# Kernel optimization log

Hardware: AMD Instinct MI355X
Metric: run time of the kernel (lower is better)

Reference implementation:

```python
import jax, jax.numpy as jnp
import numpy as np

B, S1, S2, H = 8, 2048, 2048, 1024

def setup_inputs() -> dict:
    key = jax.random.key(0)
    k1, k2, kw, kb = jax.random.split(key, 4)
    hidden1 = jax.random.normal(k1, (B, S1, H), dtype=jnp.float32)
    hidden2 = jax.random.normal(k2, (B, S2, H), dtype=jnp.float32)
    W = jax.random.normal(kw, (H, H), dtype=jnp.float32) * 0.001
    bias = jax.random.normal(kb, (1,), dtype=jnp.float32) * 0.02
    return {"hidden1": hidden1, "hidden2": hidden2, "W": W, "bias": bias}

def reference(hidden1, hidden2, W, bias):
    # weight[b, i, j] = (hidden1 @ W)[b, i, :] . hidden2[b, j, :] + bias
    weight = jnp.einsum('bih,hk,bjk->bij', hidden1, W, hidden2) + bias[0]  # (B, S1, S2)
    # softmax over s1 (dim=1), then transpose-bmm with hidden1 -> (B, S2, H)
    a1 = jax.nn.softmax(weight, axis=1)
    hidden_1 = jnp.einsum('bij,bih->bjh', a1, hidden1)
    # softmax over s2 (dim=2), bmm with hidden2 -> (B, S1, H)
    a2 = jax.nn.softmax(weight, axis=2)
    hidden_2 = jnp.einsum('bij,bjh->bih', a2, hidden2)
    return (hidden_1, hidden_2)
```

## Files before the change

### kernel.cpp

```cpp
#include <hip/hip_runtime.h>
#include <stdint.h>

#define B_  8
#define S1_ 2048
#define S2_ 2048
#define H_  1024

typedef __attribute__((ext_vector_type(8))) short bf16x8;
typedef __attribute__((ext_vector_type(4))) float f32x4;
typedef unsigned short u16;

__device__ __forceinline__ u16 f2bf(float f){
  union { float f; uint32_t v; } x; x.f = f;
  uint32_t r = x.v + 0x7fffu + ((x.v >> 16) & 1u);
  return (u16)(r >> 16);
}
__device__ __forceinline__ u16 f2h(float f){
  union { _Float16 h; u16 u; } c; c.h = (_Float16)f; return c.u;
}
__device__ __forceinline__ float h2f(u16 u){
  union { _Float16 h; u16 u; } c; c.u = u; return (float)c.h;
}
__device__ __forceinline__ uint32_t pk2bf(float lo, float hi){
  uint32_t r;
  asm("v_cvt_pk_bf16_f32 %0, %1, %2" : "=v"(r) : "v"(lo), "v"(hi));
  return r;
}
__device__ __forceinline__ void async16(void* lds, const void* g){
  __builtin_amdgcn_global_load_lds(
      (const __attribute__((address_space(1))) uint32_t*)g,
      (__attribute__((address_space(3))) uint32_t*)lds, 16, 0, 0);
}

__global__ __launch_bounds__(256) void k_cvt_bf16(const float* __restrict__ in,
                                                  u16* __restrict__ out, long n){
  long i = ((long)blockIdx.x * 256 + threadIdx.x) * 8;
  const long stride = (long)gridDim.x * 256 * 8;
  for (; i < n; i += stride){
    float4 a = *(const float4*)(in + i);
    float4 b = *(const float4*)(in + i + 4);
    union { bf16x8 v; uint32_t w[4]; } o;
    o.w[0] = pk2bf(a.x, a.y); o.w[1] = pk2bf(a.z, a.w);
    o.w[2] = pk2bf(b.x, b.y); o.w[3] = pk2bf(b.z, b.w);
    *(bf16x8*)(out + i) = o.v;
  }
}

__global__ __launch_bounds__(256) void k_tcvt(const float* __restrict__ in,
                                              u16* __restrict__ out, int R, int Cc){
  __shared__ u16 t[32][33];
  in  += (long)blockIdx.z * R * Cc;
  out += (long)blockIdx.z * R * Cc;
  const int x = threadIdx.x & 31, y0 = threadIdx.x >> 5;
  const int bx = blockIdx.x * 32, by = blockIdx.y * 32;
  for (int r = y0; r < 32; r += 8) t[r][x] = f2bf(in[(long)(by + r) * Cc + bx + x]);
  __syncthreads();
  for (int r = y0; r < 32; r += 8) out[(long)(bx + r) * R + by + x] = t[x][r];
}

__global__ __launch_bounds__(256) void k_cvtT2(const float* __restrict__ in,
                                               u16* __restrict__ out_n,
                                               u16* __restrict__ out_t, int R, int Cc){
  __shared__ u16 t[64][68];
  in    += (long)blockIdx.z * R * Cc;
  out_n += (long)blockIdx.z * R * Cc;
  out_t += (long)blockIdx.z * R * Cc;
  const int tid = threadIdx.x;
  const int r0 = tid >> 4;
  const int c4 = (tid & 15) * 4;
  const int bx = blockIdx.x * 64;
  const int by = blockIdx.y * 64;
#pragma unroll
  for (int it = 0; it < 4; ++it){
    const int r = it*16 + r0;
    float4 v = *(const float4*)(in + (long)(by + r)*Cc + bx + c4);
    u16 b0 = f2bf(v.x), b1 = f2bf(v.y), b2 = f2bf(v.z), b3 = f2bf(v.w);
    ushort4 o; o.x = b0; o.y = b1; o.z = b2; o.w = b3;
    *(ushort4*)(out_n + (long)(by + r)*Cc + bx + c4) = o;
    t[r][c4] = b0; t[r][c4+1] = b1; t[r][c4+2] = b2; t[r][c4+3] = b3;
  }
  __syncthreads();
#pragma unroll
  for (int it = 0; it < 4; ++it){
    const int c = it*16 + r0;
    ushort4 o;
    o.x = t[c4  ][c]; o.y = t[c4+1][c]; o.z = t[c4+2][c]; o.w = t[c4+3][c];
    *(ushort4*)(out_t + (long)(bx + c)*R + by + c4) = o;
  }
}

__global__ __launch_bounds__(256) void k_cvtT2m(
    const float* __restrict__ in1, u16* __restrict__ n1, u16* __restrict__ t1,
    const float* __restrict__ in2, u16* __restrict__ n2, u16* __restrict__ t2,
    int R, int Cc){
  __shared__ u16 t[64][68];
  const int zb = blockIdx.z & 7;
  const bool second = blockIdx.z >= 8;
  const float* in = (second ? in2 : in1) + (long)zb * R * Cc;
  u16* out_n = (second ? n2 : n1) + (long)zb * R * Cc;
  u16* out_t = (second ? t2 : t1) + (long)zb * R * Cc;
  const int tid = threadIdx.x;
  const int r0 = tid >> 4;
  const int c4 = (tid & 15) * 4;
  const int bx = blockIdx.x * 64;
  const int by = blockIdx.y * 64;
#pragma unroll
  for (int it = 0; it < 4; ++it){
    const int r = it*16 + r0;
    float4 v = *(const float4*)(in + (long)(by + r)*Cc + bx + c4);
    u16 b0 = f2bf(v.x), b1 = f2bf(v.y), b2 = f2bf(v.z), b3 = f2bf(v.w);
    ushort4 o; o.x = b0; o.y = b1; o.z = b2; o.w = b3;
    *(ushort4*)(out_n + (long)(by + r)*Cc + bx + c4) = o;
    t[r][c4] = b0; t[r][c4+1] = b1; t[r][c4+2] = b2; t[r][c4+3] = b3;
  }
  __syncthreads();
#pragma unroll
  for (int it = 0; it < 4; ++it){
    const int c = it*16 + r0;
    ushort4 o;
    o.x = t[c4  ][c]; o.y = t[c4+1][c]; o.z = t[c4+2][c]; o.w = t[c4+3][c];
    *(ushort4*)(out_t + (long)(bx + c)*R + by + c4) = o;
  }
}

template<int OM, bool STATS>
__global__ __launch_bounds__(512) void k_gemm256(
    const u16* __restrict__ A, const u16* __restrict__ Bm, void* __restrict__ Cv,
    int M, int N, int K, long sA, long sB, long sC,
    float* __restrict__ rpmax, float* __restrict__ rpsum,
    float* __restrict__ cpmax, float* __restrict__ cpsum)
{
  const int GX = gridDim.x, GY = gridDim.y;
  const long plane = (long)GX * GY;
  const long tot = plane * gridDim.z;
  const long lin = blockIdx.x + (long)GX * (blockIdx.y + (long)GY * blockIdx.z);
  const long chunk = tot >> 3;
  const long swz = (lin & 7) * chunk + (lin >> 3);
  const int bz = (int)(swz / plane);
  const int rr = (int)(swz % plane);
  const int by_ = rr / GX, bx_ = rr % GX;

  A += (long)bz * sA; Bm += (long)bz * sB;
  __shared__ u16 lds[2 * 32768];
  const int tid = threadIdx.x, lane = tid & 63, w = tid >> 6;
  const int wm = w >> 2, wn = w & 3;
  const int brow = bx_ * 256, bcol = by_ * 256;

  f32x4 acc[8][4];
#pragma unroll
  for (int m=0;m<8;++m)
#pragma unroll
    for (int n=0;n<4;++n) acc[m][n] = (f32x4){0.f,0.f,0.f,0.f};

  const int fr = lane & 15;
  const int hi = lane >> 4;
  const int sk0 = (((0*4)+hi) ^ (fr & 7)) * 8;
  const int sk1 = (((1*4)+hi) ^ (fr & 7)) * 8;

  const u16* gAs[4]; const u16* gBs[4];
#pragma unroll
  for (int j=0;j<4;++j){
    const int cc = (w*4 + j)*64 + lane;
    const int row = cc >> 3;
    const int sl = (cc & 7) ^ (row & 7);
    gAs[j] = A  + (long)(brow + row) * K + sl*8;
    gBs[j] = Bm + (long)(bcol + row) * K + sl*8;
  }
  auto stage = [&](int buf, int t){
    u16* base = lds + buf*32768;
#pragma unroll
    for (int j=0;j<4;++j) async16(base + (w*4+j)*512, gAs[j] + (long)t*64);
#pragma unroll
    for (int j=0;j<4;++j) async16(base + 16384 + (w*4+j)*512, gBs[j] + (long)t*64);
  };
  auto ldfragK = [&](int buf, int sk, bf16x8* a, bf16x8* b){
    const u16* At = lds + buf*32768;
    const u16* Bt = At + 16384;
#pragma unroll
    for (int n=0;n<4;++n) b[n] = *(const bf16x8*)(Bt + (wn*64 + n*16 + fr)*64 + sk);
#pragma unroll
    for (int m=0;m<8;++m) a[m] = *(const bf16x8*)(At + (wm*128 + m*16 + fr)*64 + sk);
  };

  const int NT = K >> 6;
  stage(0, 0);
  asm volatile("s_waitcnt vmcnt(0)" ::: "memory");
  __builtin_amdgcn_s_barrier();

  for (int t = 0; t < NT; ++t){
    const int cur = t & 1;
    if (t + 1 < NT) stage(cur ^ 1, t + 1);

    bf16x8 a[8], b[4];
    ldfragK(cur, sk0, a, b);
    __builtin_amdgcn_s_setprio(1);
#pragma unroll
    for (int m=0;m<8;++m)
#pragma unroll
      for (int n=0;n<4;++n)
        acc[m][n] = __builtin_amdgcn_mfma_f32_16x16x32_bf16(a[m], b[n], acc[m][n], 0,0,0);
    __builtin_amdgcn_s_setprio(0);

    ldfragK(cur, sk1, a, b);
    __builtin_amdgcn_s_setprio(1);
#pragma unroll
    for (int m=0;m<8;++m)
#pragma unroll
      for (int n=0;n<4;++n)
        acc[m][n] = __builtin_amdgcn_mfma_f32_16x16x32_bf16(a[m], b[n], acc[m][n], 0,0,0);
    __builtin_amdgcn_s_setprio(0);

    if (t + 1 < NT){
      asm volatile("s_waitcnt vmcnt(0)" ::: "memory");
      asm volatile("s_waitcnt lgkmcnt(0)" ::: "memory");
      __builtin_amdgcn_s_barrier();
    }
  }

  const int crow = brow + wm*128 + hi * 4;
  const int ccol = bcol + wn*64 + fr;
  if constexpr (OM == 2){
    float* C = (float*)Cv + (long)bz * sC;
#pragma unroll
    for (int m=0;m<8;++m)
#pragma unroll
      for (int n=0;n<4;++n){
        f32x4 v = acc[m][n];
        float* cp = C + (long)(crow + m*16) * N + ccol + n*16;
#pragma unroll
        for (int q=0;q<4;++q) cp[(long)q*N] = v[q];
      }
  } else {
    u16* C = (u16*)Cv + (long)bz * sC;
#pragma unroll
    for (int m=0;m<8;++m)
#pragma unroll
      for (int n=0;n<4;++n){
        f32x4 v = acc[m][n];
        u16* cp = C + (long)(crow + m*16) * N + ccol + n*16;
#pragma unroll
        for (int q=0;q<4;++q) cp[(long)q*N] = OM ? f2h(v[q]) : f2bf(v[q]);
      }
  }

  if constexpr (STATS){
#pragma unroll
    for (int m=0;m<8;++m){
      f32x4 mx = acc[m][0];
#pragma unroll
      for (int n=1;n<4;++n)
#pragma unroll
        for (int q=0;q<4;++q) mx[q] = fmaxf(mx[q], acc[m][n][q]);
#pragma unroll
      for (int off=1; off<16; off<<=1)
#pragma unroll
        for (int q=0;q<4;++q) mx[q] = fmaxf(mx[q], __shfl_xor(mx[q], off));
      f32x4 sm = (f32x4){0.f,0.f,0.f,0.f};
#pragma unroll
      for (int n=0;n<4;++n)
#pragma unroll
        for (int q=0;q<4;++q) sm[q] += __expf(acc[m][n][q] - mx[q]);
#pragma unroll
      for (int off=1; off<16; off<<=1)
#pragma unroll
        for (int q=0;q<4;++q) sm[q] += __shfl_xor(sm[q], off);
      if (fr == 0){
        const int nb = by_*4 + wn;
        const long rb = ((long)bz*32 + nb)*2048 + brow + wm*128 + m*16 + hi*4;
#pragma unroll
        for (int q=0;q<4;++q){ rpmax[rb+q] = mx[q]; rpsum[rb+q] = sm[q]; }
      }
    }
#pragma unroll
    for (int n=0;n<4;++n){
      float mx = acc[0][n][0];
#pragma unroll
      for (int m=0;m<8;++m)
#pragma unroll
        for (int q=0;q<4;++q) mx = fmaxf(mx, acc[m][n][q]);
      mx = fmaxf(mx, __shfl_xor(mx, 16));
      mx = fmaxf(mx, __shfl_xor(mx, 32));
      float sm = 0.f;
#pragma unroll
      for (int m=0;m<8;++m)
#pragma unroll
        for (int q=0;q<4;++q) sm += __expf(acc[m][n][q] - mx);
      sm += __shfl_xor(sm, 16);
      sm += __shfl_xor(sm, 32);
      if (hi == 0){
        const int mb = bx_*2 + wm;
        const long cb = ((long)bz*16 + mb)*2048 + bcol + wn*64 + n*16 + fr;
        cpmax[cb] = mx; cpsum[cb] = sm;
      }
    }
  }
}

__global__ __launch_bounds__(256) void k_combine(
    const float* __restrict__ rpmax, const float* __restrict__ rpsum,
    const float* __restrict__ cpmax, const float* __restrict__ cpsum,
    float* __restrict__ rmax, float* __restrict__ rinv,
    float* __restrict__ cmax, float* __restrict__ cinv)
{
  const long i = (long)blockIdx.x*256 + threadIdx.x;
  const int b = (int)(i >> 11), r = (int)(i & 2047);
  if (blockIdx.y == 0){
    const float* pm = rpmax + ((long)b*32)*2048 + r;
    const float* ps = rpsum + ((long)b*32)*2048 + r;
    float m = -3.4e38f;
#pragma unroll
    for (int k=0;k<32;++k) m = fmaxf(m, pm[(long)k*2048]);
    float s = 0.f;
#pragma unroll
    for (int k=0;k<32;++k) s += ps[(long)k*2048] * __expf(pm[(long)k*2048] - m);
    rmax[i] = m; rinv[i] = 1.f / s;
  } else {
    const float* pm = cpmax + ((long)b*16)*2048 + r;
    const float* ps = cpsum + ((long)b*16)*2048 + r;
    float m = -3.4e38f;
#pragma unroll
    for (int k=0;k<16;++k) m = fmaxf(m, pm[(long)k*2048]);
    float s = 0.f;
#pragma unroll
    for (int k=0;k<16;++k) s += ps[(long)k*2048] * __expf(pm[(long)k*2048] - m);
    cmax[i] = m; cinv[i] = 1.f / s;
  }
}

__global__ __launch_bounds__(256) void k_p1t2(u16* __restrict__ Wg, u16* __restrict__ P2,
                                              const float* __restrict__ cmax,
                                              const float* __restrict__ cinv,
                                              const float* __restrict__ rmax,
                                              const float* __restrict__ rinv){
  const int ti = blockIdx.x, tj = blockIdx.y;
  if (tj < ti) return;
  const int b = blockIdx.z;
  u16* S = Wg + (long)b * S1_ * S2_;
  u16* P2b = P2 ? P2 + (long)b * S1_ * S2_ : (u16*)nullptr;
  const int I0 = ti*64, J0 = tj*64;
  __shared__ u16 tA[64][68];
  __shared__ u16 tB[64][68];
  __shared__ float scm[128], sci[128];
  const int tid = threadIdx.x;
  if (tid < 64){ scm[tid] = cmax[b*S2_ + J0 + tid]; sci[tid] = cinv[b*S2_ + J0 + tid]; }
  else if (tid < 128){ scm[tid] = cmax[b*S2_ + I0 + tid - 64]; sci[tid] = cinv[b*S2_ + I0 + tid - 64]; }
  __syncthreads();

  const int r0 = tid >> 3;
  const int c8 = (tid & 7) * 8;
#pragma unroll
  for (int it = 0; it < 2; ++it){
    const int r = it*32 + r0;
    bf16x8 v = *(const bf16x8*)(S + (long)(I0 + r)*S2_ + J0 + c8);
    const float rm = rmax[b*S1_ + I0 + r], ri = rinv[b*S1_ + I0 + r];
    union { bf16x8 v; uint32_t w[4]; } p2o;
#pragma unroll
    for (int k=0;k<4;++k){
      float x0 = h2f((u16)v[2*k]), x1 = h2f((u16)v[2*k+1]);
      p2o.w[k] = pk2bf(__expf(x0 - rm)*ri, __expf(x1 - rm)*ri);
      tA[r][c8+2*k]   = f2bf(__expf(x0 - scm[c8+2*k])   * sci[c8+2*k]);
      tA[r][c8+2*k+1] = f2bf(__expf(x1 - scm[c8+2*k+1]) * sci[c8+2*k+1]);
    }
    if (P2b) *(bf16x8*)(P2b + (long)(I0 + r)*S2_ + J0 + c8) = p2o.v;
  }
  if (ti != tj){
#pragma unroll
    for (int it = 0; it < 2; ++it){
      const int r = it*32 + r0;
      bf16x8 v = *(const bf16x8*)(S + (long)(J0 + r)*S2_ + I0 + c8);
      const float rm = rmax[b*S1_ + J0 + r], ri = rinv[b*S1_ + J0 + r];
      union { bf16x8 v; uint32_t w[4]; } p2o;
#pragma unroll
      for (int k=0;k<4;++k){
        float x0 = h2f((u16)v[2*k]), x1 = h2f((u16)v[2*k+1]);
        p2o.w[k] = pk2bf(__expf(x0 - rm)*ri, __expf(x1 - rm)*ri);
        tB[r][c8+2*k]   = f2bf(__expf(x0 - scm[64+c8+2*k])   * sci[64+c8+2*k]);
        tB[r][c8+2*k+1] = f2bf(__expf(x1 - scm[64+c8+2*k+1]) * sci[64+c8+2*k+1]);
      }
      if (P2b) *(bf16x8*)(P2b + (long)(J0 + r)*S2_ + I0 + c8) = p2o.v;
    }
  }
  __syncthreads();
  const int rr = tid >> 4;
  const int c4 = (tid & 15) * 4;
#pragma unroll
  for (int it = 0; it < 4; ++it){
    const int c = it*16 + rr;
    ushort4 o;
    o.x = tA[c4  ][c]; o.y = tA[c4+1][c]; o.z = tA[c4+2][c]; o.w = tA[c4+3][c];
    *(ushort4*)(S + (long)(J0 + c)*S2_ + I0 + c4) = o;
  }
  if (ti != tj){
#pragma unroll
    for (int it = 0; it < 4; ++it){
      const int c = it*16 + rr;
      ushort4 o;
      o.x = tB[c4  ][c]; o.y = tB[c4+1][c]; o.z = tB[c4+2][c]; o.w = tB[c4+3][c];
      *(ushort4*)(S + (long)(I0 + c)*S2_ + J0 + c4) = o;
    }
  }
}

__global__ __launch_bounds__(256) void k_gemm_h2(
    const u16* __restrict__ Wg, const u16* __restrict__ Bt, float* __restrict__ C,
    const float* __restrict__ rmax, const float* __restrict__ rinv)
{
  const int b = blockIdx.z;
  const u16* A  = Wg + (long)b * S1_ * S2_;
  const u16* Bp = Bt + (long)b * H_ * S2_;
  float* Cp = C + (long)b * S1_ * H_;

  __shared__ u16 As[128*32];
  __shared__ u16 Bs[128*32];
  const int tid = threadIdx.x, lane = tid & 63, w = tid >> 6;
  const int wr = (w >> 1) * 64, wc = (w & 1) * 64;
  const int brow = blockIdx.x * 128, bcol = blockIdx.y * 128;
  f32x4 acc[4][4];
#pragma unroll
  for (int m=0;m<4;++m)
#pragma unroll
    for (int n=0;n<4;++n) acc[m][n] = (f32x4){0.f,0.f,0.f,0.f};

  const int arow = w*16 + (lane >> 2);
  const int scol = (lane & 3) * 8;
  const u16* gA0 = A + (long)(brow + arow) * S2_ + scol;
  const u16* gA1 = gA0 + (long)64 * S2_;
  const float rm0 = rmax[b*S1_ + brow + arow],      ri0 = rinv[b*S1_ + brow + arow];
  const float rm1 = rmax[b*S1_ + brow + arow + 64], ri1 = rinv[b*S1_ + brow + arow + 64];
  u16* wA0 = As + arow*32 + scol;
  u16* wA1 = As + (arow+64)*32 + scol;

  const u16* gb = Bp + (long)(bcol + arow) * S2_ + scol;
  u16* lB0 = Bs + (w*16)*32;  u16* lB1 = Bs + (64 + w*16)*32;

  const int koff = (lane >> 4) * 8;
  const int fr = lane & 15;

  for (int k0 = 0; k0 < S2_; k0 += 32){
    bf16x8 x0 = *(const bf16x8*)(gA0 + k0);
    bf16x8 x1 = *(const bf16x8*)(gA1 + k0);
    async16(lB0, gb);  async16(lB1, gb + (long)64*S2_);
    gb += 32;
    union { bf16x8 v; uint32_t w4[4]; } y0, y1;
#pragma unroll
    for (int k=0;k<4;++k){
      y0.w4[k] = pk2bf(__expf(h2f((u16)x0[2*k])   - rm0) * ri0,
                       __expf(h2f((u16)x0[2*k+1]) - rm0) * ri0);
      y1.w4[k] = pk2bf(__expf(h2f((u16)x1[2*k])   - rm1) * ri1,
                       __expf(h2f((u16)x1[2*k+1]) - rm1) * ri1);
    }
    *(bf16x8*)wA0 = y0.v;
    *(bf16x8*)wA1 = y1.v;
    __syncthreads();
    bf16x8 af[4], bf[4];
#pragma unroll
    for (int m=0;m<4;++m) af[m] = *(const bf16x8*)(As + (wr + m*16 + fr)*32 + koff);
#pragma unroll
    for (int n=0;n<4;++n) bf[n] = *(const bf16x8*)(Bs + (wc + n*16 + fr)*32 + koff);
#pragma unroll
    for (int m=0;m<4;++m)
#pragma unroll
      for (int n=0;n<4;++n)
        acc[m][n] = __builtin_amdgcn_mfma_f32_16x16x32_bf16(af[m], bf[n], acc[m][n], 0,0,0);
    __syncthreads();
  }
  const int crow = brow + wr + (lane >> 4) * 4;
  const int ccol = bcol + wc + fr;
#pragma unroll
  for (int m=0;m<4;++m)
#pragma unroll
    for (int n=0;n<4;++n){
      f32x4 v = acc[m][n];
      float* cp = Cp + (long)(crow + m*16) * H_ + ccol + n*16;
#pragma unroll
      for (int q=0;q<4;++q) cp[(long)q*H_] = v[q];
    }
}

extern "C" void kernel_launch(void* const* d_in, const int* in_sizes, int n_in,
                              void* d_out, int out_size, void* d_ws, size_t ws_size,
                              hipStream_t stream)
{
  const float* h1 = (const float*)d_in[0];
  const float* h2 = (const float*)d_in[1];
  const float* W  = (const float*)d_in[2];
  float* out0 = (float*)d_out;
  float* out1 = out0 + (size_t)B_ * S2_ * H_;

  const long NE = (long)B_ * S1_ * H_;
  const long NS = (long)B_ * S1_ * S2_;

  char* ws = (char*)d_ws;
  size_t off = 0;
  float* rmax = (float*)(ws + off); off += (size_t)B_*S1_*4;
  float* rinv = (float*)(ws + off); off += (size_t)B_*S1_*4;
  float* cmax = (float*)(ws + off); off += (size_t)B_*S2_*4;
  float* cinv = (float*)(ws + off); off += (size_t)B_*S2_*4;
  u16* Wg  = (u16*)(ws + off);
  u16* WTb = Wg;
  off += (size_t)NS*2;
  u16* h1t = (u16*)(ws + off); off += (size_t)NE*2;

  const bool use_p2 = ws_size >= off + (size_t)NS*2;
  u16* P2 = use_p2 ? (u16*)(ws + off) : (u16*)nullptr;
  size_t off2 = off + (use_p2 ? (size_t)NS*2 : 0);
  const bool ws_h2t = ws_size >= off2 + (size_t)NE*2;

  u16* h1b = (u16*)out0;
  u16* h2b = (u16*)out0 + NE;
  u16* h2t = ws_h2t ? (u16*)(ws + off2) : (u16*)out0;
  u16* Qb  = (u16*)out1;
  float* rpmax = (float*)((u16*)out1 + NE);
  float* rpsum = rpmax + (size_t)B_*32*2048;
  float* cpmax = rpsum + (size_t)B_*32*2048;
  float* cpsum = cpmax + (size_t)B_*16*2048;

  if (ws_h2t){
    k_cvtT2m<<<dim3(16,32,16), 256, 0, stream>>>(h1, h1b, h1t, h2, h2b, h2t, S1_, H_);
  } else {
    k_cvtT2<<<dim3(16,32,8), 256, 0, stream>>>(h1, h1b, h1t, S1_, H_);
    k_cvt_bf16<<<dim3(4096), 256, 0, stream>>>(h2, h2b, NE);
  }
  k_tcvt<<<dim3(32,32,1), 256, 0, stream>>>(W, WTb, H_, H_);
  k_gemm256<0,false><<<dim3(8, 4, 8), 512, 0, stream>>>(h1b, WTb, Qb, S1_, H_, H_,
        (long)S1_*H_, 0L, (long)S1_*H_, nullptr, nullptr, nullptr, nullptr);
  if (!ws_h2t){
    k_tcvt<<<dim3(32,64,8), 256, 0, stream>>>(h2, h2t, S2_, H_);
  }
  k_gemm256<1,true><<<dim3(8, 8, 8), 512, 0, stream>>>(Qb, h2b, Wg, S1_, S2_, H_,
        (long)S1_*H_, (long)S2_*H_, (long)S1_*S2_, rpmax, rpsum, cpmax, cpsum);
  k_combine<<<dim3(64, 2), 256, 0, stream>>>(rpmax, rpsum, cpmax, cpsum,
                                             rmax, rinv, cmax, cinv);
  if (use_p2){
    k_p1t2<<<dim3(32,32,8), 256, 0, stream>>>(Wg, P2, cmax, cinv, rmax, rinv);
    k_gemm256<2,false><<<dim3(8, 4, 8), 512, 0, stream>>>(P2, h2t, out1, S1_, H_, S2_,
          (long)S1_*S2_, (long)H_*S2_, (long)S1_*H_, nullptr, nullptr, nullptr, nullptr);
  } else {
    k_gemm_h2<<<dim3(16, 8, 8), 256, 0, stream>>>(Wg, h2t, out1, rmax, rinv);
    k_p1t2<<<dim3(32,32,8), 256, 0, stream>>>(Wg, (u16*)nullptr, cmax, cinv, rmax, rinv);
  }
  k_gemm256<2,false><<<dim3(8, 4, 8), 512, 0, stream>>>(Wg, h1t, out0, S2_, H_, S1_,
        (long)S1_*S2_, (long)H_*S1_, (long)S2_*H_, nullptr, nullptr, nullptr, nullptr);
}
```

Measured before the change: 355.2 us.

## Add 256x128-tile triple-buffered GEMM kernel for the H-output GEMMs

Adds a new GEMM kernel that uses a 256x128 output tile with 4x4 MFMA fragments per wave, a three-stage async LDS pipeline, and an XCD-aware block swizzle. The Q projection GEMM and both P@H output GEMMs now use it instead of the 256x256 kernel, which doubles the grid to 512 blocks. The aim is better CU occupancy and load balance across the 256 CUs, since the old grid of 256 blocks left none to spare. In exchange, each block loads more A-tile traffic per output element because reuse along N is lower.

```diff
diff --git a/kernel.cpp b/kernel.cpp
--- a/kernel.cpp
+++ b/kernel.cpp
@@ -293,6 +293,117 @@
         cpmax[cb] = mx; cpsum[cb] = sm;
       }
     }
+  }
+}
+
+template<int OM>
+__global__ __launch_bounds__(512, 4) void k_gemm128n(
+    const u16* __restrict__ A, const u16* __restrict__ Bm, void* __restrict__ Cv,
+    int M, int N, int K, long sA, long sB, long sC)
+{
+  const int GX = gridDim.x, GY = gridDim.y;
+  const long plane = (long)GX * GY;
+  const long tot = plane * gridDim.z;
+  const long lin = blockIdx.x + (long)GX * (blockIdx.y + (long)GY * blockIdx.z);
+  const long chunk = tot >> 3;
+  const long swz = (lin & 7) * chunk + (lin >> 3);
+  const int bz = (int)(swz / plane);
+  const int rr = (int)(swz % plane);
+  const int by_ = rr / GX, bx_ = rr % GX;
+
+  A += (long)bz * sA; Bm += (long)bz * sB;
+  __shared__ u16 lds[3 * 12288];
+  const int tid = threadIdx.x, lane = tid & 63, w = tid >> 6;
+  const int wm = w >> 1, wn = w & 1;
+  const int brow = bx_ * 256, bcol = by_ * 128;
+
+  f32x4 acc[4][4];
+#pragma unroll
+  for (int m=0;m<4;++m)
+#pragma unroll
+    for (int n=0;n<4;++n) acc[m][n] = (f32x4){0.f,0.f,0.f,0.f};
+
+  const int fr = lane & 15;
+  const int hi = lane >> 4;
+  const int g8s = (hi ^ ((lane >> 1) & 3)) * 8;
+
+  const int cc0 = w*128 + lane;
+  const int cc1 = w*128 + 64 + lane;
+  const int ccb = w*64 + lane;
+  const int sl0 = (cc0 & 3) ^ ((cc0 >> 3) & 3);
+  const int sl1 = (cc1 & 3) ^ ((cc1 >> 3) & 3);
+  const int slb = (ccb & 3) ^ ((ccb >> 3) & 3);
+  const u16* gA0 = A  + (long)(brow + (cc0 >> 2)) * K + sl0*8;
+  const u16* gA1 = A  + (long)(brow + (cc1 >> 2)) * K + sl1*8;
+  const u16* gB0 = Bm + (long)(bcol + (ccb >> 2)) * K + slb*8;
+  const int dA0 = (w*128)*8, dA1 = (w*128 + 64)*8, dB0 = 8192 + (w*64)*8;
+
+  auto stage = [&](int buf, int t){
+    u16* base = lds + buf*12288;
+    async16(base + dA0, gA0 + (long)t*32);
+    async16(base + dA1, gA1 + (long)t*32);
+    async16(base + dB0, gB0 + (long)t*32);
+  };
+  auto ldfrag = [&](int buf, bf16x8* a, bf16x8* b){
+    const u16* At = lds + buf*12288;
+    const u16* Bt = At + 8192;
+#pragma unroll
+    for (int n=0;n<4;++n) b[n] = *(const bf16x8*)(Bt + (wn*64 + n*16 + fr)*32 + g8s);
+#pragma unroll
+    for (int m=0;m<4;++m) a[m] = *(const bf16x8*)(At + (wm*64 + m*16 + fr)*32 + g8s);
+  };
+
+  const int NT = K >> 5;
+  stage(0, 0); stage(1, 1);
+  asm volatile("s_waitcnt vmcnt(0)" ::: "memory");
+  __builtin_amdgcn_s_barrier();
+
+  for (int t = 0; t < NT; ++t){
+    const int cur = t % 3;
+    if (t + 2 < NT) stage((t + 2) % 3, t + 2);
+
+    bf16x8 a[4], b[4];
+    ldfrag(cur, a, b);
+    __builtin_amdgcn_s_setprio(1);
+#pragma unroll
+    for (int m=0;m<4;++m)
+#pragma unroll
+      for (int n=0;n<4;++n)
+        acc[m][n] = __builtin_amdgcn_mfma_f32_16x16x32_bf16(a[m], b[n], acc[m][n], 0,0,0);
+    __builtin_amdgcn_s_setprio(0);
+
+    if (t + 1 < NT){
+      if (t + 2 < NT) asm volatile("s_waitcnt vmcnt(3)" ::: "memory");
+      else            asm volatile("s_waitcnt vmcnt(0)" ::: "memory");
+      asm volatile("s_waitcnt lgkmcnt(0)" ::: "memory");
+      __builtin_amdgcn_s_barrier();
+    }
+  }
+
+  const int crow = brow + wm*64 + hi * 4;
+  const int ccol = bcol + wn*64 + fr;
+  if constexpr (OM == 2){
+    float* C = (float*)Cv + (long)bz * sC;
+#pragma unroll
+    for (int m=0;m<4;++m)
+#pragma unroll
+      for (int n=0;n<4;++n){
+        f32x4 v = acc[m][n];
+        float* cp = C + (long)(crow + m*16) * N + ccol + n*16;
+#pragma unroll
+        for (int q=0;q<4;++q) cp[(long)q*N] = v[q];
+      }
+  } else {
+    u16* C = (u16*)Cv + (long)bz * sC;
+#pragma unroll
+    for (int m=0;m<4;++m)
+#pragma unroll
+      for (int n=0;n<4;++n){
+        f32x4 v = acc[m][n];
+        u16* cp = C + (long)(crow + m*16) * N + ccol + n*16;
+#pragma unroll
+        for (int q=0;q<4;++q) cp[(long)q*N] = OM ? f2h(v[q]) : f2bf(v[q]);
+      }
   }
 }
 
@@ -522,8 +633,8 @@
     k_cvt_bf16<<<dim3(4096), 256, 0, stream>>>(h2, h2b, NE);
   }
   k_tcvt<<<dim3(32,32,1), 256, 0, stream>>>(W, WTb, H_, H_);
-  k_gemm256<0,false><<<dim3(8, 4, 8), 512, 0, stream>>>(h1b, WTb, Qb, S1_, H_, H_,
-        (long)S1_*H_, 0L, (long)S1_*H_, nullptr, nullptr, nullptr, nullptr);
+  k_gemm128n<0><<<dim3(8, 8, 8), 512, 0, stream>>>(h1b, WTb, Qb, S1_, H_, H_,
+        (long)S1_*H_, 0L, (long)S1_*H_);
   if (!ws_h2t){
     k_tcvt<<<dim3(32,64,8), 256, 0, stream>>>(h2, h2t, S2_, H_);
   }
@@ -533,12 +644,12 @@
                                              rmax, rinv, cmax, cinv);
   if (use_p2){
     k_p1t2<<<dim3(32,32,8), 256, 0, stream>>>(Wg, P2, cmax, cinv, rmax, rinv);
-    k_gemm256<2,false><<<dim3(8, 4, 8), 512, 0, stream>>>(P2, h2t, out1, S1_, H_, S2_,
-          (long)S1_*S2_, (long)H_*S2_, (long)S1_*H_, nullptr, nullptr, nullptr, nullptr);
+    k_gemm128n<2><<<dim3(8, 8, 8), 512, 0, stream>>>(P2, h2t, out1, S1_, H_, S2_,
+          (long)S1_*S2_, (long)H_*S2_, (long)S1_*H_);
   } else {
     k_gemm_h2<<<dim3(16, 8, 8), 256, 0, stream>>>(Wg, h2t, out1, rmax, rinv);
     k_p1t2<<<dim3(32,32,8), 256, 0, stream>>>(Wg, (u16*)nullptr, cmax, cinv, rmax, rinv);
   }
-  k_gemm256<2,false><<<dim3(8, 4, 8), 512, 0, stream>>>(Wg, h1t, out0, S2_, H_, S1_,
-        (long)S1_*S2_, (long)H_*S1_, (long)S2_*H_, nullptr, nullptr, nullptr, nullptr);
-}
+  k_gemm128n<2><<<dim3(8, 8, 8), 512, 0, stream>>>(Wg, h1t, out0, S2_, H_, S1_,
+        (long)S1_*S2_, (long)H_*S1_, (long)S2_*H_);
+}
```

Result: slower. 385.1 us (+8.4%).
